# Kernel tuning notes

Measured on AMD Instinct MI355X. Metric: run time of the kernel, lower is better.

## Reference

```python
import jax, jax.numpy as jnp
import numpy as np

EPS = 1e-5

def bn_eval(x, p):
    # p: [4, C] = gamma, beta, running_mean, running_var; channel-last broadcast
    g, b, m, v = p[0], p[1], p[2], p[3]
    return (x - m) * (g / jnp.sqrt(v + EPS)) + b

def _bn_params(k, c):
    k1, k2, k3, k4 = jax.random.split(k, 4)
    gamma = jax.random.uniform(k1, (c,)) + 0.5
    beta = jax.random.normal(k2, (c,)) * 0.1
    mean = jax.random.normal(k3, (c,)) * 0.1
    var = jax.random.uniform(k4, (c,)) + 0.5
    return jnp.stack([gamma, beta, mean, var])

def _lin(k, fan_in, fan_out):
    bound = 1.0 / np.sqrt(fan_in)
    kw, kb = jax.random.split(k)
    w = jax.random.uniform(kw, (fan_in, fan_out), minval=-bound, maxval=bound)
    b = jax.random.uniform(kb, (fan_out,), minval=-bound, maxval=bound)
    return w, b

def setup_inputs() -> dict:
    key = jax.random.key(0)
    B, N, S, C, G = 2, 4096, 16, 256, 8
    ks = jax.random.split(key, 20)
    feats = jax.random.normal(ks[0], (B, N, C), dtype=jnp.float32)
    coords = jax.random.normal(ks[1], (B, N, 3), dtype=jnp.float32)
    index = jax.random.randint(ks[2], (B, N, S), 0, N, dtype=jnp.int32)
    wq, bq = _lin(ks[3], C, C); bnq = _bn_params(ks[4], C)
    wk, bk = _lin(ks[5], C, C); bnk = _bn_params(ks[6], C)
    wv, bv = _lin(ks[7], C, C)
    pm_w1, pm_b1 = _lin(ks[8], 3, C); pm_bn = _bn_params(ks[9], C)
    pm_w2, pm_b2 = _lin(ks[10], C, C)
    pb_w1, pb_b1 = _lin(ks[11], 3, C); pb_bn = _bn_params(ks[12], C)
    pb_w2, pb_b2 = _lin(ks[13], C, C)
    we_w1, we_b1 = _lin(ks[14], C, G); we_bn = _bn_params(ks[15], G)
    we_w2, we_b2 = _lin(ks[16], G, G)
    return dict(feats=feats, coords=coords, index=index,
                wq=wq, bq=bq, bnq=bnq, wk=wk, bk=bk, bnk=bnk, wv=wv, bv=bv,
                pm_w1=pm_w1, pm_b1=pm_b1, pm_bn=pm_bn, pm_w2=pm_w2, pm_b2=pm_b2,
                pb_w1=pb_w1, pb_b1=pb_b1, pb_bn=pb_bn, pb_w2=pb_w2, pb_b2=pb_b2,
                we_w1=we_w1, we_b1=we_b1, we_bn=we_bn, we_w2=we_w2, we_b2=we_b2)

def reference(feats, coords, index,
              wq, bq, bnq, wk, bk, bnk, wv, bv,
              pm_w1, pm_b1, pm_bn, pm_w2, pm_b2,
              pb_w1, pb_b1, pb_bn, pb_w2, pb_b2,
              we_w1, we_b1, we_bn, we_w2, we_b2):
    B, N, C = feats.shape
    S = index.shape[2]
    G = we_w1.shape[1]
    q = jax.nn.relu(bn_eval(feats @ wq + bq, bnq))                       # [B,N,C]
    k = jax.nn.relu(bn_eval(feats @ wk + bk, bnk))                       # [B,N,C]
    v = feats @ wv + bv                                                   # [B,N,C]
    idx = index.reshape(B, N * S)
    key_g = jnp.take_along_axis(k, idx[:, :, None], axis=1).reshape(B, N, S, C)
    val_g = jnp.take_along_axis(v, idx[:, :, None], axis=1).reshape(B, N, S, C)
    crd_g = jnp.take_along_axis(coords, idx[:, :, None], axis=1).reshape(B, N, S, 3)
    relation_qk = key_g - q[:, :, None, :]                                # [B,N,S,C]
    pos = coords[:, :, None, :] - crd_g                                   # [B,N,S,3]
    pem = jax.nn.relu(bn_eval(pos @ pm_w1 + pm_b1, pm_bn)) @ pm_w2 + pm_b2
    relation_qk = relation_qk * pem
    peb = jax.nn.relu(bn_eval(pos @ pb_w1 + pb_b1, pb_bn)) @ pb_w2 + pb_b2
    relation_qk = relation_qk + peb
    val_g = val_g + peb
    w = jax.nn.relu(bn_eval(relation_qk @ we_w1 + we_b1, we_bn)) @ we_w2 + we_b2  # [B,N,S,G]
    w = jax.nn.softmax(w, axis=2)                                         # softmax over neighbors
    val_g = val_g.reshape(B, N, S, G, C // G)
    out = jnp.einsum('bnsgi,bnsg->bngi', val_g, w).reshape(B, N, C)
    return out
```

## Files before the change

### kernel.cpp

```cpp
#include <hip/hip_runtime.h>


typedef __attribute__((ext_vector_type(8))) short bf16x8_t;
typedef __attribute__((ext_vector_type(4))) float f32x4_t;

#define BN_EPS 1e-5f

__device__ __forceinline__ float b2f(unsigned int b) {
    union { unsigned int u; float f; } x; x.u = b << 16; return x.f;
}
__device__ __forceinline__ float blo(unsigned int v) {
    union { unsigned int u; float f; } x; x.u = v << 16; return x.f;
}
__device__ __forceinline__ float bhi(unsigned int v) {
    union { unsigned int u; float f; } x; x.u = v & 0xffff0000u; return x.f;
}
__device__ __forceinline__ unsigned int fbits(float f) {
    union { float f; unsigned int u; } x; x.f = f; return x.u;
}
__device__ __forceinline__ unsigned short f2b(float f) {
    unsigned int u = fbits(f);
    return (unsigned short)((u + 0x7fffu + ((u >> 16) & 1u)) >> 16);
}
__device__ __forceinline__ unsigned int f2bpk(float a, float b) {
    unsigned int ua = fbits(a), ub = fbits(b);
    unsigned int ta = ua + 0x7fffu + ((ua >> 16) & 1u);
    unsigned int tb = ub + 0x7fffu + ((ub >> 16) & 1u);
    return (ta >> 16) | (tb & 0xffff0000u);
}
__device__ __forceinline__ unsigned int relpair(unsigned int kb, unsigned int qb,
                                                unsigned int pm_, unsigned int pb_) {
    float r0 = (blo(kb) - blo(qb)) * blo(pm_) + blo(pb_);
    float r1 = (bhi(kb) - bhi(qb)) * bhi(pm_) + bhi(pb_);
    return f2bpk(r0, r1);
}

__global__ __launch_bounds__(256) void k_prep(
    const float* __restrict__ wq, const float* __restrict__ wk,
    const float* __restrict__ wv, const float* __restrict__ pm2,
    const float* __restrict__ pb2, unsigned short* __restrict__ wsT)
{
    __shared__ unsigned short T[32][72];
    const int bid = blockIdx.x;
    const int mat = bid >> 5;
    const int kk  = (bid >> 2) & 7;
    const int ntq = bid & 3;
    const float* s = (mat == 0) ? wq : (mat == 1) ? wk : (mat == 2) ? wv
                     : (mat == 3) ? pm2 : pb2;
    const int t = threadIdx.x;
    {
        int c = t & 63, r0 = t >> 6;
        for (int i = 0; i < 8; ++i) {
            int r = r0 + i * 4;
            T[r][c] = f2b(s[(kk * 32 + r) * 256 + ntq * 64 + c]);
        }
    }
    __syncthreads();
    {
        int seg = t >> 6, lane = t & 63;
        int col = seg * 16 + (lane & 15);
        int kr  = (lane >> 4) * 8;
        unsigned int v[8];
        #pragma unroll
        for (int j = 0; j < 8; ++j) v[j] = T[kr + j][col];
        uint4 o;
        o.x = v[0] | (v[1] << 16);
        o.y = v[2] | (v[3] << 16);
        o.z = v[4] | (v[5] << 16);
        o.w = v[6] | (v[7] << 16);
        *(uint4*)(wsT + mat * 65536 + (ntq * 4 + seg) * 4096 + kk * 512 + lane * 8) = o;
    }
}

__global__ __launch_bounds__(256) void k_qkv(
    const float* __restrict__ feats,
    const unsigned short* __restrict__ wT,
    const float* __restrict__ bq, const float* __restrict__ bnq,
    const float* __restrict__ bk, const float* __restrict__ bnk,
    const float* __restrict__ bv,
    unsigned short* __restrict__ qkv)
{
    __shared__ unsigned short A[32][264];
    const int t    = threadIdx.x;
    const int widx = blockIdx.x >> 8;
    const int mb   = blockIdx.x & 255;

    for (int i = 0; i < 8; ++i) {
        int row = 4 * i + (t >> 6), col = (t & 63) * 4;
        float4 f = *(const float4*)(feats + (mb * 32 + row) * 256 + col);
        *(uint2*)&A[row][col] = make_uint2(f2bpk(f.x, f.y), f2bpk(f.z, f.w));
    }
    __syncthreads();

    const int lane = t & 63, w = t >> 6;
    const int ln15 = lane & 15, quad = lane >> 4;
    const int mt = w & 1, nh = w >> 1;

    bf16x8_t afr[8];
    #pragma unroll
    for (int kk = 0; kk < 8; ++kk)
        afr[kk] = *(const bf16x8_t*)&A[mt * 16 + ln15][kk * 32 + quad * 8];

    const unsigned short* W = wT + widx * 65536;
    const float* bias = (widx == 0) ? bq : (widx == 1) ? bk : bv;
    const float* bn   = (widx == 0) ? bnq : (widx == 1) ? bnk : nullptr;
    unsigned short* dst = qkv + (size_t)widx * 8192 * 256;

    const f32x4_t fzero = {0.f, 0.f, 0.f, 0.f};
    f32x4_t acc[8];
    for (int j = 0; j < 8; ++j) acc[j] = fzero;

    #pragma unroll
    for (int kk = 0; kk < 8; ++kk) {
        #pragma unroll
        for (int j = 0; j < 8; ++j) {
            int nt = nh * 8 + j;
            bf16x8_t bfr = *(const bf16x8_t*)(W + ((nt * 8 + kk) * 64 + lane) * 8);
            acc[j] = __builtin_amdgcn_mfma_f32_16x16x32_bf16(afr[kk], bfr, acc[j], 0, 0, 0);
        }
    }

    float bb[8], sc[8], mu[8], be[8];
    #pragma unroll
    for (int j = 0; j < 8; ++j) {
        int c = (nh * 8 + j) * 16 + ln15;
        bb[j] = bias[c];
        if (bn) {
            sc[j] = bn[c] / sqrtf(bn[768 + c] + BN_EPS);
            be[j] = bn[256 + c];
            mu[j] = bn[512 + c];
        }
    }
    __syncthreads();
    #pragma unroll
    for (int j = 0; j < 8; ++j) {
        int c = (nh * 8 + j) * 16 + ln15;
        float y[4];
        for (int r = 0; r < 4; ++r) {
            y[r] = acc[j][r] + bb[j];
            if (bn) y[r] = fmaxf((y[r] - mu[j]) * sc[j] + be[j], 0.f);
        }
        for (int r = 0; r < 4; r += 2) {
            unsigned int pk = f2bpk(y[r], y[r + 1]);
            A[mt * 16 + quad * 4 + r][c]     = (unsigned short)pk;
            A[mt * 16 + quad * 4 + r + 1][c] = (unsigned short)(pk >> 16);
        }
    }
    __syncthreads();
    {
        int row = t >> 3, cc = (t & 7) * 32;
        #pragma unroll
        for (int j = 0; j < 4; ++j) {
            uint4 v = *(const uint4*)&A[row][cc + 8 * j];
            *(uint4*)(dst + (mb * 32 + row) * 256 + cc + 8 * j) = v;
        }
    }
}

__global__ __launch_bounds__(256, 2) void k_main(
    const float* __restrict__ coords,
    const int*   __restrict__ index,
    const unsigned short* __restrict__ qm,
    const unsigned short* __restrict__ km,
    const unsigned short* __restrict__ vm,
    const unsigned short* __restrict__ pmw2F,
    const unsigned short* __restrict__ pbw2F,
    const float* __restrict__ pm_w1, const float* __restrict__ pm_b1,
    const float* __restrict__ pm_bn, const float* __restrict__ pm_b2,
    const float* __restrict__ pb_w1, const float* __restrict__ pb_b1,
    const float* __restrict__ pb_bn, const float* __restrict__ pb_b2,
    const float* __restrict__ we_w1, const float* __restrict__ we_b1,
    const float* __restrict__ we_bn, const float* __restrict__ we_w2,
    const float* __restrict__ we_b2,
    float* __restrict__ out)
{
    __shared__ unsigned short bufR[64][264];
    __shared__ unsigned short bufP[64][264];
    __shared__ __align__(16) char uni[8448];
    float (*Wpm)[256] = (float(*)[256])uni;
    float (*Wpb)[256] = (float(*)[256])(uni + 4096);
    unsigned short (*we1T)[264] = (unsigned short(*)[264])uni;
    float (*us_)[8] = (float(*)[8])(uni + 4224);
    float (*lg_)[8] = (float(*)[8])(uni + 6272);
    __shared__ float posA[64][4];
    __shared__ float bias2[2][256];
    __shared__ float swe[8], dwe[8], web2[8];
    __shared__ float we2s[8][8];

    const int t  = threadIdx.x;
    const int P0 = blockIdx.x * 4;
    const int b  = P0 >> 12;

    const int m3  = t >> 2;
    const int Pg3 = P0 + (m3 >> 4);
    const int rg3 = (b << 12) + index[Pg3 * 16 + (m3 & 15)];
    const int c3  = (t & 3) * 8;
    uint4 kpre[8];
    {
        const unsigned short* krow = km + rg3 * 256 + c3;
        #pragma unroll
        for (int i = 0; i < 8; ++i) kpre[i] = *(const uint4*)(krow + 32 * i);
    }
    const int p5 = t >> 6, c5 = (t & 63) * 4;
    uint2 vpre[16];
    #pragma unroll
    for (int s = 0; s < 16; ++s) {
        int rgv = (b << 12) + index[(P0 + p5) * 16 + s];
        vpre[s] = *(const uint2*)(vm + rgv * 256 + c5);
    }

    if (t < 64) {
        int p = t >> 4, s = t & 15;
        int Pg = P0 + p;
        int rg = (b << 12) + index[Pg * 16 + s];
        posA[t][0] = coords[Pg * 3 + 0] - coords[rg * 3 + 0];
        posA[t][1] = coords[Pg * 3 + 1] - coords[rg * 3 + 1];
        posA[t][2] = coords[Pg * 3 + 2] - coords[rg * 3 + 2];
        posA[t][3] = 0.f;
    }
    {
        int c = t;
        float sc = pm_bn[c] / sqrtf(pm_bn[768 + c] + BN_EPS);
        Wpm[0][c] = pm_w1[c] * sc;
        Wpm[1][c] = pm_w1[256 + c] * sc;
        Wpm[2][c] = pm_w1[512 + c] * sc;
        Wpm[3][c] = (pm_b1[c] - pm_bn[512 + c]) * sc + pm_bn[256 + c];
        sc = pb_bn[c] / sqrtf(pb_bn[768 + c] + BN_EPS);
        Wpb[0][c] = pb_w1[c] * sc;
        Wpb[1][c] = pb_w1[256 + c] * sc;
        Wpb[2][c] = pb_w1[512 + c] * sc;
        Wpb[3][c] = (pb_b1[c] - pb_bn[512 + c]) * sc + pb_bn[256 + c];
        bias2[0][c] = pb_b2[c];
        bias2[1][c] = pm_b2[c];
    }
    if (t < 8) {
        float sc = we_bn[t] / sqrtf(we_bn[24 + t] + BN_EPS);
        swe[t]  = sc;
        dwe[t]  = (we_b1[t] - we_bn[16 + t]) * sc + we_bn[8 + t];
        web2[t] = we_b2[t];
    }
    if (t < 64) we2s[t >> 3][t & 7] = we_w2[t];
    __syncthreads();

    const int lane = t & 63, w = t >> 6;
    const int ln15 = lane & 15, quad = lane >> 4;
    const int mrow = w * 16 + ln15;
    const f32x4_t fzero = {0.f, 0.f, 0.f, 0.f};

    const int hc = (t & 127) * 2;
    const int hm0 = (t >> 7) * 32;

    {
        float w00 = Wpb[0][hc], w01 = Wpb[0][hc + 1];
        float w10 = Wpb[1][hc], w11 = Wpb[1][hc + 1];
        float w20 = Wpb[2][hc], w21 = Wpb[2][hc + 1];
        float w30 = Wpb[3][hc], w31 = Wpb[3][hc + 1];
        for (int i = 0; i < 32; ++i) {
            int m = hm0 + i;
            float4 p = *(const float4*)&posA[m][0];
            float h0 = fmaxf(p.x * w00 + p.y * w10 + p.z * w20 + w30, 0.f);
            float h1 = fmaxf(p.x * w01 + p.y * w11 + p.z * w21 + w31, 0.f);
            *(unsigned int*)&bufR[m][hc] = f2bpk(h0, h1);
        }
    }
    __syncthreads();

    f32x4_t acc[4][4];
    for (int a = 0; a < 4; ++a) for (int mt = 0; mt < 4; ++mt) acc[a][mt] = fzero;
    #pragma unroll
    for (int kk = 0; kk < 8; ++kk) {
        bf16x8_t afr[4];
        #pragma unroll
        for (int mt = 0; mt < 4; ++mt)
            afr[mt] = *(const bf16x8_t*)&bufR[mt * 16 + ln15][kk * 32 + quad * 8];
        #pragma unroll
        for (int ntl = 0; ntl < 4; ++ntl) {
            int nt = w * 4 + ntl;
            bf16x8_t bfr = *(const bf16x8_t*)(pbw2F + ((nt * 8 + kk) * 64 + lane) * 8);
            #pragma unroll
            for (int mt = 0; mt < 4; ++mt)
                acc[ntl][mt] = __builtin_amdgcn_mfma_f32_16x16x32_bf16(afr[mt], bfr, acc[ntl][mt], 0, 0, 0);
        }
    }
    __syncthreads();
    #pragma unroll
    for (int ntl = 0; ntl < 4; ++ntl) {
        int c = (w * 4 + ntl) * 16 + ln15;
        float bb = bias2[0][c];
        for (int mt = 0; mt < 4; ++mt)
            for (int r = 0; r < 4; r += 2) {
                unsigned int pk = f2bpk(acc[ntl][mt][r] + bb, acc[ntl][mt][r + 1] + bb);
                bufP[mt * 16 + quad * 4 + r][c]     = (unsigned short)pk;
                bufP[mt * 16 + quad * 4 + r + 1][c] = (unsigned short)(pk >> 16);
            }
    }
    {
        float w00 = Wpm[0][hc], w01 = Wpm[0][hc + 1];
        float w10 = Wpm[1][hc], w11 = Wpm[1][hc + 1];
        float w20 = Wpm[2][hc], w21 = Wpm[2][hc + 1];
        float w30 = Wpm[3][hc], w31 = Wpm[3][hc + 1];
        for (int i = 0; i < 32; ++i) {
            int m = hm0 + i;
            float4 p = *(const float4*)&posA[m][0];
            float h0 = fmaxf(p.x * w00 + p.y * w10 + p.z * w20 + w30, 0.f);
            float h1 = fmaxf(p.x * w01 + p.y * w11 + p.z * w21 + w31, 0.f);
            *(unsigned int*)&bufR[m][hc] = f2bpk(h0, h1);
        }
    }
    __syncthreads();

    for (int a = 0; a < 4; ++a) for (int mt = 0; mt < 4; ++mt) acc[a][mt] = fzero;
    #pragma unroll
    for (int kk = 0; kk < 8; ++kk) {
        bf16x8_t afr[4];
        #pragma unroll
        for (int mt = 0; mt < 4; ++mt)
            afr[mt] = *(const bf16x8_t*)&bufR[mt * 16 + ln15][kk * 32 + quad * 8];
        #pragma unroll
        for (int ntl = 0; ntl < 4; ++ntl) {
            int nt = w * 4 + ntl;
            bf16x8_t bfr = *(const bf16x8_t*)(pmw2F + ((nt * 8 + kk) * 64 + lane) * 8);
            #pragma unroll
            for (int mt = 0; mt < 4; ++mt)
                acc[ntl][mt] = __builtin_amdgcn_mfma_f32_16x16x32_bf16(afr[mt], bfr, acc[ntl][mt], 0, 0, 0);
        }
    }
    __syncthreads();
    #pragma unroll
    for (int ntl = 0; ntl < 4; ++ntl) {
        int c = (w * 4 + ntl) * 16 + ln15;
        float bb = bias2[1][c];
        for (int mt = 0; mt < 4; ++mt)
            for (int r = 0; r < 4; r += 2) {
                unsigned int pk = f2bpk(acc[ntl][mt][r] + bb, acc[ntl][mt][r + 1] + bb);
                bufR[mt * 16 + quad * 4 + r][c]     = (unsigned short)pk;
                bufR[mt * 16 + quad * 4 + r + 1][c] = (unsigned short)(pk >> 16);
            }
    }
    __syncthreads();

    if (t < 64) {
        int g = t >> 3, j8 = t & 7;
        for (int i = 0; i < 32; ++i) {
            int c = j8 * 32 + i;
            we1T[g][c] = f2b(we_w1[c * 8 + g]);
        }
    }
    {
        const unsigned short* qrow = qm + Pg3 * 256 + c3;
        #pragma unroll
        for (int i = 0; i < 8; ++i) {
            int c = c3 + 32 * i;
            uint4 qb  = *(const uint4*)(qrow + 32 * i);
            uint4 pmv = *(const uint4*)&bufR[m3][c];
            uint4 pbv = *(const uint4*)&bufP[m3][c];
            uint4 r;
            r.x = relpair(kpre[i].x, qb.x, pmv.x, pbv.x);
            r.y = relpair(kpre[i].y, qb.y, pmv.y, pbv.y);
            r.z = relpair(kpre[i].z, qb.z, pmv.z, pbv.z);
            r.w = relpair(kpre[i].w, qb.w, pmv.w, pbv.w);
            *(uint4*)&bufR[m3][c] = r;
        }
    }
    __syncthreads();

    {
        const bf16x8_t bz = {0, 0, 0, 0, 0, 0, 0, 0};
        f32x4_t lacc = fzero;
        #pragma unroll
        for (int kk = 0; kk < 8; ++kk) {
            bf16x8_t afr = *(const bf16x8_t*)&bufR[mrow][kk * 32 + quad * 8];
            bf16x8_t bfr = bz;
            if (ln15 < 8) bfr = *(const bf16x8_t*)&we1T[ln15][kk * 32 + quad * 8];
            lacc = __builtin_amdgcn_mfma_f32_16x16x32_bf16(afr, bfr, lacc, 0, 0, 0);
        }
        if (ln15 < 8) {
            float sc = swe[ln15], dd = dwe[ln15];
            for (int r = 0; r < 4; ++r)
                us_[w * 16 + quad * 4 + r][ln15] = fmaxf(lacc[r] * sc + dd, 0.f);
        }
    }
    __syncthreads();

    if (t < 64) {
        float uv[8];
        for (int gp = 0; gp < 8; ++gp) uv[gp] = us_[t][gp];
        for (int g = 0; g < 8; ++g) {
            float l = web2[g];
            for (int gp = 0; gp < 8; ++gp) l += uv[gp] * we2s[gp][g];
            lg_[t][g] = l;
        }
    }
    __syncthreads();

    if (t < 32) {
        int p = t >> 3, g = t & 7;
        float mx = -1e30f;
        for (int s = 0; s < 16; ++s) mx = fmaxf(mx, lg_[p * 16 + s][g]);
        float e[16], sum = 0.f;
        for (int s = 0; s < 16; ++s) { e[s] = __expf(lg_[p * 16 + s][g] - mx); sum += e[s]; }
        float inv = 1.f / sum;
        for (int s = 0; s < 16; ++s) lg_[p * 16 + s][g] = e[s] * inv;
    }
    __syncthreads();

    {
        int g = c5 >> 5;
        float a0 = 0.f, a1 = 0.f, a2 = 0.f, a3 = 0.f;
        #pragma unroll
        for (int s = 0; s < 16; ++s) {
            int m = p5 * 16 + s;
            float wv_ = lg_[m][g];
            uint2 v4 = vpre[s];
            uint2 p4 = *(const uint2*)&bufP[m][c5];
            a0 += wv_ * (blo(v4.x) + blo(p4.x));
            a1 += wv_ * (bhi(v4.x) + bhi(p4.x));
            a2 += wv_ * (blo(v4.y) + blo(p4.y));
            a3 += wv_ * (bhi(v4.y) + bhi(p4.y));
        }
        *(float4*)(out + (size_t)(P0 + p5) * 256 + c5) = make_float4(a0, a1, a2, a3);
    }
}

extern "C" void kernel_launch(void* const* d_in, const int* in_sizes, int n_in,
                              void* d_out, int out_size, void* d_ws, size_t ws_size,
                              hipStream_t stream)
{
    const float* feats  = (const float*)d_in[0];
    const float* coords = (const float*)d_in[1];
    const int*   index  = (const int*)d_in[2];
    const float* wq     = (const float*)d_in[3];
    const float* bq     = (const float*)d_in[4];
    const float* bnq    = (const float*)d_in[5];
    const float* wk     = (const float*)d_in[6];
    const float* bk     = (const float*)d_in[7];
    const float* bnk    = (const float*)d_in[8];
    const float* wv     = (const float*)d_in[9];
    const float* bv     = (const float*)d_in[10];
    const float* pm_w1  = (const float*)d_in[11];
    const float* pm_b1  = (const float*)d_in[12];
    const float* pm_bn  = (const float*)d_in[13];
    const float* pm_w2  = (const float*)d_in[14];
    const float* pm_b2  = (const float*)d_in[15];
    const float* pb_w1  = (const float*)d_in[16];
    const float* pb_b1  = (const float*)d_in[17];
    const float* pb_bn  = (const float*)d_in[18];
    const float* pb_w2  = (const float*)d_in[19];
    const float* pb_b2  = (const float*)d_in[20];
    const float* we_w1  = (const float*)d_in[21];
    const float* we_b1  = (const float*)d_in[22];
    const float* we_bn  = (const float*)d_in[23];
    const float* we_w2  = (const float*)d_in[24];
    const float* we_b2  = (const float*)d_in[25];

    unsigned short* qkv = (unsigned short*)d_ws;
    unsigned short* wsT = qkv + (size_t)3 * 8192 * 256;

    const size_t need = ((size_t)3 * 8192 * 256 + (size_t)5 * 65536) * 2;
    if (ws_size < need) {
        hipMemsetAsync(d_out, 0, (size_t)out_size * 4, stream);
        return;
    }

    k_prep<<<160,  256, 0, stream>>>(wq, wk, wv, pm_w2, pb_w2, wsT);
    k_qkv <<<768,  256, 0, stream>>>(feats, wsT, bq, bnq, bk, bnk, bv, qkv);
    k_main<<<2048, 256, 0, stream>>>(coords, index,
                                     qkv,
                                     qkv + (size_t)8192 * 256,
                                     qkv + (size_t)2 * 8192 * 256,
                                     wsT + 3 * 65536,
                                     wsT + 4 * 65536,
                                     pm_w1, pm_b1, pm_bn, pm_b2,
                                     pb_w1, pb_b1, pb_bn, pb_b2,
                                     we_w1, we_b1, we_bn, we_w2, we_b2,
                                     (float*)d_out);
}
```

Measured before the change: 230.2 us.

## Precompute folded BN weights in prep kernel and make k_main tail wave-local

The folded BN first-layer weights and the transposed bf16 we_w1 are now computed once in extra k_prep blocks and stored in the workspace, so each k_main block no longer rebuilds them in shared memory. Work in k_main is regrouped so each wave owns one point's 16 neighbor rows. The relation computation feeds the MFMA directly from registers instead of going through a shared-memory round trip. The softmax and aggregation tail uses wave-local lgkmcnt waits instead of block barriers, and the value gather moves from an upfront register prefetch to loads inside the final loop. This cuts per-block setup, barriers and register pressure, at the cost of loads that are less overlapped and reliance on the waitcnt being enough for intra-wave LDS ordering.

```diff
diff --git a/kernel.cpp b/kernel.cpp
--- a/kernel.cpp
+++ b/kernel.cpp
@@ -5,10 +5,8 @@
 typedef __attribute__((ext_vector_type(4))) float f32x4_t;
 
 #define BN_EPS 1e-5f
-
-__device__ __forceinline__ float b2f(unsigned int b) {
-    union { unsigned int u; float f; } x; x.u = b << 16; return x.f;
-}
+#define WSYNC() asm volatile("s_waitcnt lgkmcnt(0)" ::: "memory")
+
 __device__ __forceinline__ float blo(unsigned int v) {
     union { unsigned int u; float f; } x; x.u = v << 16; return x.f;
 }
@@ -38,37 +36,61 @@
 __global__ __launch_bounds__(256) void k_prep(
     const float* __restrict__ wq, const float* __restrict__ wk,
     const float* __restrict__ wv, const float* __restrict__ pm2,
-    const float* __restrict__ pb2, unsigned short* __restrict__ wsT)
+    const float* __restrict__ pb2,
+    const float* __restrict__ pm_w1, const float* __restrict__ pm_b1,
+    const float* __restrict__ pm_bn,
+    const float* __restrict__ pb_w1, const float* __restrict__ pb_b1,
+    const float* __restrict__ pb_bn,
+    const float* __restrict__ we_w1,
+    unsigned short* __restrict__ wsT, float* __restrict__ W4,
+    unsigned short* __restrict__ we1TF)
 {
-    __shared__ unsigned short T[32][72];
-    const int bid = blockIdx.x;
-    const int mat = bid >> 5;
-    const int kk  = (bid >> 2) & 7;
-    const int ntq = bid & 3;
-    const float* s = (mat == 0) ? wq : (mat == 1) ? wk : (mat == 2) ? wv
-                     : (mat == 3) ? pm2 : pb2;
-    const int t = threadIdx.x;
-    {
-        int c = t & 63, r0 = t >> 6;
-        for (int i = 0; i < 8; ++i) {
-            int r = r0 + i * 4;
-            T[r][c] = f2b(s[(kk * 32 + r) * 256 + ntq * 64 + c]);
-        }
-    }
-    __syncthreads();
-    {
-        int seg = t >> 6, lane = t & 63;
-        int col = seg * 16 + (lane & 15);
-        int kr  = (lane >> 4) * 8;
-        unsigned int v[8];
-        #pragma unroll
-        for (int j = 0; j < 8; ++j) v[j] = T[kr + j][col];
-        uint4 o;
-        o.x = v[0] | (v[1] << 16);
-        o.y = v[2] | (v[3] << 16);
-        o.z = v[4] | (v[5] << 16);
-        o.w = v[6] | (v[7] << 16);
-        *(uint4*)(wsT + mat * 65536 + (ntq * 4 + seg) * 4096 + kk * 512 + lane * 8) = o;
+    const int bid = blockIdx.x, t = threadIdx.x;
+    if (bid < 160) {
+        __shared__ unsigned short T[32][72];
+        const int mat = bid >> 5;
+        const int kk  = (bid >> 2) & 7;
+        const int ntq = bid & 3;
+        const float* s = (mat == 0) ? wq : (mat == 1) ? wk : (mat == 2) ? wv
+                         : (mat == 3) ? pm2 : pb2;
+        {
+            int c = t & 63, r0 = t >> 6;
+            for (int i = 0; i < 8; ++i) {
+                int r = r0 + i * 4;
+                T[r][c] = f2b(s[(kk * 32 + r) * 256 + ntq * 64 + c]);
+            }
+        }
+        __syncthreads();
+        {
+            int seg = t >> 6, lane = t & 63;
+            int col = seg * 16 + (lane & 15);
+            int kr  = (lane >> 4) * 8;
+            unsigned int v[8];
+            #pragma unroll
+            for (int j = 0; j < 8; ++j) v[j] = T[kr + j][col];
+            uint4 o;
+            o.x = v[0] | (v[1] << 16);
+            o.y = v[2] | (v[3] << 16);
+            o.z = v[4] | (v[5] << 16);
+            o.w = v[6] | (v[7] << 16);
+            *(uint4*)(wsT + mat * 65536 + (ntq * 4 + seg) * 4096 + kk * 512 + lane * 8) = o;
+        }
+    } else if (bid == 160) {
+        int c = t;
+        float s = pm_bn[c] / sqrtf(pm_bn[768 + c] + BN_EPS);
+        float4 wm = make_float4(pm_w1[c] * s, pm_w1[256 + c] * s, pm_w1[512 + c] * s,
+                                (pm_b1[c] - pm_bn[512 + c]) * s + pm_bn[256 + c]);
+        s = pb_bn[c] / sqrtf(pb_bn[768 + c] + BN_EPS);
+        float4 wb = make_float4(pb_w1[c] * s, pb_w1[256 + c] * s, pb_w1[512 + c] * s,
+                                (pb_b1[c] - pb_bn[512 + c]) * s + pb_bn[256 + c]);
+        ((float4*)W4)[c]       = wm;
+        ((float4*)W4)[256 + c] = wb;
+    } else {
+        for (int j = 0; j < 8; ++j) {
+            int e = t * 8 + j;
+            int g = e >> 8, c = e & 255;
+            we1TF[g * 256 + c] = f2b(we_w1[c * 8 + g]);
+        }
     }
 }
 
@@ -165,103 +187,68 @@
     const unsigned short* __restrict__ vm,
     const unsigned short* __restrict__ pmw2F,
     const unsigned short* __restrict__ pbw2F,
-    const float* __restrict__ pm_w1, const float* __restrict__ pm_b1,
-    const float* __restrict__ pm_bn, const float* __restrict__ pm_b2,
-    const float* __restrict__ pb_w1, const float* __restrict__ pb_b1,
-    const float* __restrict__ pb_bn, const float* __restrict__ pb_b2,
-    const float* __restrict__ we_w1, const float* __restrict__ we_b1,
-    const float* __restrict__ we_bn, const float* __restrict__ we_w2,
-    const float* __restrict__ we_b2,
+    const float* __restrict__ W4,
+    const unsigned short* __restrict__ we1TF,
+    const float* __restrict__ pm_b2, const float* __restrict__ pb_b2,
+    const float* __restrict__ we_b1, const float* __restrict__ we_bn,
+    const float* __restrict__ we_w2, const float* __restrict__ we_b2,
     float* __restrict__ out)
 {
     __shared__ unsigned short bufR[64][264];
     __shared__ unsigned short bufP[64][264];
-    __shared__ __align__(16) char uni[8448];
-    float (*Wpm)[256] = (float(*)[256])uni;
-    float (*Wpb)[256] = (float(*)[256])(uni + 4096);
-    unsigned short (*we1T)[264] = (unsigned short(*)[264])uni;
-    float (*us_)[8] = (float(*)[8])(uni + 4224);
-    float (*lg_)[8] = (float(*)[8])(uni + 6272);
     __shared__ float posA[64][4];
-    __shared__ float bias2[2][256];
-    __shared__ float swe[8], dwe[8], web2[8];
+    __shared__ float us_[64][8];
+    __shared__ int   rowg_[64];
     __shared__ float we2s[8][8];
+    __shared__ float web2[8];
 
     const int t  = threadIdx.x;
     const int P0 = blockIdx.x * 4;
-    const int b  = P0 >> 12;
-
-    const int m3  = t >> 2;
-    const int Pg3 = P0 + (m3 >> 4);
-    const int rg3 = (b << 12) + index[Pg3 * 16 + (m3 & 15)];
-    const int c3  = (t & 3) * 8;
+    const int bb_ = P0 >> 12;
+    const int w = t >> 6, lane = t & 63;
+    const int ln15 = lane & 15, quad = lane >> 4;
+    const int R0 = w * 16;
+    const int Pg = P0 + w;
+
+    const int rg = (bb_ << 12) + index[Pg * 16 + ln15];
     uint4 kpre[8];
-    {
-        const unsigned short* krow = km + rg3 * 256 + c3;
-        #pragma unroll
-        for (int i = 0; i < 8; ++i) kpre[i] = *(const uint4*)(krow + 32 * i);
-    }
-    const int p5 = t >> 6, c5 = (t & 63) * 4;
-    uint2 vpre[16];
-    #pragma unroll
-    for (int s = 0; s < 16; ++s) {
-        int rgv = (b << 12) + index[(P0 + p5) * 16 + s];
-        vpre[s] = *(const uint2*)(vm + rgv * 256 + c5);
-    }
-
-    if (t < 64) {
-        int p = t >> 4, s = t & 15;
-        int Pg = P0 + p;
-        int rg = (b << 12) + index[Pg * 16 + s];
-        posA[t][0] = coords[Pg * 3 + 0] - coords[rg * 3 + 0];
-        posA[t][1] = coords[Pg * 3 + 1] - coords[rg * 3 + 1];
-        posA[t][2] = coords[Pg * 3 + 2] - coords[rg * 3 + 2];
-        posA[t][3] = 0.f;
-    }
-    {
-        int c = t;
-        float sc = pm_bn[c] / sqrtf(pm_bn[768 + c] + BN_EPS);
-        Wpm[0][c] = pm_w1[c] * sc;
-        Wpm[1][c] = pm_w1[256 + c] * sc;
-        Wpm[2][c] = pm_w1[512 + c] * sc;
-        Wpm[3][c] = (pm_b1[c] - pm_bn[512 + c]) * sc + pm_bn[256 + c];
-        sc = pb_bn[c] / sqrtf(pb_bn[768 + c] + BN_EPS);
-        Wpb[0][c] = pb_w1[c] * sc;
-        Wpb[1][c] = pb_w1[256 + c] * sc;
-        Wpb[2][c] = pb_w1[512 + c] * sc;
-        Wpb[3][c] = (pb_b1[c] - pb_bn[512 + c]) * sc + pb_bn[256 + c];
-        bias2[0][c] = pb_b2[c];
-        bias2[1][c] = pm_b2[c];
-    }
-    if (t < 8) {
-        float sc = we_bn[t] / sqrtf(we_bn[24 + t] + BN_EPS);
-        swe[t]  = sc;
-        dwe[t]  = (we_b1[t] - we_bn[16 + t]) * sc + we_bn[8 + t];
-        web2[t] = we_b2[t];
+    #pragma unroll
+    for (int kk = 0; kk < 8; ++kk)
+        kpre[kk] = *(const uint4*)(km + rg * 256 + kk * 32 + quad * 8);
+
+    const int hc = lane * 4;
+    float4 cm[4], cb[4];
+    #pragma unroll
+    for (int i = 0; i < 4; ++i) {
+        cm[i] = ((const float4*)W4)[hc + i];
+        cb[i] = ((const float4*)W4)[256 + hc + i];
+    }
+
+    const int g8 = ln15 & 7;
+    const float swe_r = we_bn[g8] / sqrtf(we_bn[24 + g8] + BN_EPS);
+    const float dwe_r = (we_b1[g8] - we_bn[16 + g8]) * swe_r + we_bn[8 + g8];
+
+    if (lane < 16) {
+        rowg_[R0 + lane] = rg;
+        posA[R0 + lane][0] = coords[Pg * 3 + 0] - coords[rg * 3 + 0];
+        posA[R0 + lane][1] = coords[Pg * 3 + 1] - coords[rg * 3 + 1];
+        posA[R0 + lane][2] = coords[Pg * 3 + 2] - coords[rg * 3 + 2];
+        posA[R0 + lane][3] = 0.f;
     }
     if (t < 64) we2s[t >> 3][t & 7] = we_w2[t];
-    __syncthreads();
-
-    const int lane = t & 63, w = t >> 6;
-    const int ln15 = lane & 15, quad = lane >> 4;
-    const int mrow = w * 16 + ln15;
+    if (t < 8)  web2[t] = we_b2[t];
+    WSYNC();
+
     const f32x4_t fzero = {0.f, 0.f, 0.f, 0.f};
 
-    const int hc = (t & 127) * 2;
-    const int hm0 = (t >> 7) * 32;
-
-    {
-        float w00 = Wpb[0][hc], w01 = Wpb[0][hc + 1];
-        float w10 = Wpb[1][hc], w11 = Wpb[1][hc + 1];
-        float w20 = Wpb[2][hc], w21 = Wpb[2][hc + 1];
-        float w30 = Wpb[3][hc], w31 = Wpb[3][hc + 1];
-        for (int i = 0; i < 32; ++i) {
-            int m = hm0 + i;
-            float4 p = *(const float4*)&posA[m][0];
-            float h0 = fmaxf(p.x * w00 + p.y * w10 + p.z * w20 + w30, 0.f);
-            float h1 = fmaxf(p.x * w01 + p.y * w11 + p.z * w21 + w31, 0.f);
-            *(unsigned int*)&bufR[m][hc] = f2bpk(h0, h1);
-        }
+    #pragma unroll
+    for (int m = 0; m < 16; ++m) {
+        float4 p = *(const float4*)&posA[R0 + m][0];
+        float h0 = fmaxf(p.x * cb[0].x + p.y * cb[0].y + p.z * cb[0].z + cb[0].w, 0.f);
+        float h1 = fmaxf(p.x * cb[1].x + p.y * cb[1].y + p.z * cb[1].z + cb[1].w, 0.f);
+        float h2 = fmaxf(p.x * cb[2].x + p.y * cb[2].y + p.z * cb[2].z + cb[2].w, 0.f);
+        float h3 = fmaxf(p.x * cb[3].x + p.y * cb[3].y + p.z * cb[3].z + cb[3].w, 0.f);
+        *(uint2*)&bufR[R0 + m][hc] = make_uint2(f2bpk(h0, h1), f2bpk(h2, h3));
     }
     __syncthreads();
 
@@ -283,29 +270,26 @@
         }
     }
     __syncthreads();
+
     #pragma unroll
     for (int ntl = 0; ntl < 4; ++ntl) {
         int c = (w * 4 + ntl) * 16 + ln15;
-        float bb = bias2[0][c];
+        float bbv = pb_b2[c];
         for (int mt = 0; mt < 4; ++mt)
             for (int r = 0; r < 4; r += 2) {
-                unsigned int pk = f2bpk(acc[ntl][mt][r] + bb, acc[ntl][mt][r + 1] + bb);
+                unsigned int pk = f2bpk(acc[ntl][mt][r] + bbv, acc[ntl][mt][r + 1] + bbv);
                 bufP[mt * 16 + quad * 4 + r][c]     = (unsigned short)pk;
                 bufP[mt * 16 + quad * 4 + r + 1][c] = (unsigned short)(pk >> 16);
             }
     }
-    {
-        float w00 = Wpm[0][hc], w01 = Wpm[0][hc + 1];
-        float w10 = Wpm[1][hc], w11 = Wpm[1][hc + 1];
-        float w20 = Wpm[2][hc], w21 = Wpm[2][hc + 1];
-        float w30 = Wpm[3][hc], w31 = Wpm[3][hc + 1];
-        for (int i = 0; i < 32; ++i) {
-            int m = hm0 + i;
-            float4 p = *(const float4*)&posA[m][0];
-            float h0 = fmaxf(p.x * w00 + p.y * w10 + p.z * w20 + w30, 0.f);
-            float h1 = fmaxf(p.x * w01 + p.y * w11 + p.z * w21 + w31, 0.f);
-            *(unsigned int*)&bufR[m][hc] = f2bpk(h0, h1);
-        }
+    #pragma unroll
+    for (int m = 0; m < 16; ++m) {
+        float4 p = *(const float4*)&posA[R0 + m][0];
+        float h0 = fmaxf(p.x * cm[0].x + p.y * cm[0].y + p.z * cm[0].z + cm[0].w, 0.f);
+        float h1 = fmaxf(p.x * cm[1].x + p.y * cm[1].y + p.z * cm[1].z + cm[1].w, 0.f);
+        float h2 = fmaxf(p.x * cm[2].x + p.y * cm[2].y + p.z * cm[2].z + cm[2].w, 0.f);
+        float h3 = fmaxf(p.x * cm[3].x + p.y * cm[3].y + p.z * cm[3].z + cm[3].w, 0.f);
+        *(uint2*)&bufR[R0 + m][hc] = make_uint2(f2bpk(h0, h1), f2bpk(h2, h3));
     }
     __syncthreads();
 
@@ -326,99 +310,87 @@
         }
     }
     __syncthreads();
+
     #pragma unroll
     for (int ntl = 0; ntl < 4; ++ntl) {
         int c = (w * 4 + ntl) * 16 + ln15;
-        float bb = bias2[1][c];
+        float bbv = pm_b2[c];
         for (int mt = 0; mt < 4; ++mt)
             for (int r = 0; r < 4; r += 2) {
-                unsigned int pk = f2bpk(acc[ntl][mt][r] + bb, acc[ntl][mt][r + 1] + bb);
+                unsigned int pk = f2bpk(acc[ntl][mt][r] + bbv, acc[ntl][mt][r + 1] + bbv);
                 bufR[mt * 16 + quad * 4 + r][c]     = (unsigned short)pk;
                 bufR[mt * 16 + quad * 4 + r + 1][c] = (unsigned short)(pk >> 16);
             }
     }
     __syncthreads();
 
-    if (t < 64) {
-        int g = t >> 3, j8 = t & 7;
-        for (int i = 0; i < 32; ++i) {
-            int c = j8 * 32 + i;
-            we1T[g][c] = f2b(we_w1[c * 8 + g]);
-        }
-    }
-    {
-        const unsigned short* qrow = qm + Pg3 * 256 + c3;
-        #pragma unroll
-        for (int i = 0; i < 8; ++i) {
-            int c = c3 + 32 * i;
-            uint4 qb  = *(const uint4*)(qrow + 32 * i);
-            uint4 pmv = *(const uint4*)&bufR[m3][c];
-            uint4 pbv = *(const uint4*)&bufP[m3][c];
-            uint4 r;
-            r.x = relpair(kpre[i].x, qb.x, pmv.x, pbv.x);
-            r.y = relpair(kpre[i].y, qb.y, pmv.y, pbv.y);
-            r.z = relpair(kpre[i].z, qb.z, pmv.z, pbv.z);
-            r.w = relpair(kpre[i].w, qb.w, pmv.w, pbv.w);
-            *(uint4*)&bufR[m3][c] = r;
-        }
-    }
-    __syncthreads();
-
     {
         const bf16x8_t bz = {0, 0, 0, 0, 0, 0, 0, 0};
         f32x4_t lacc = fzero;
         #pragma unroll
         for (int kk = 0; kk < 8; ++kk) {
-            bf16x8_t afr = *(const bf16x8_t*)&bufR[mrow][kk * 32 + quad * 8];
+            int cb8 = kk * 32 + quad * 8;
+            uint4 pm4 = *(const uint4*)&bufR[R0 + ln15][cb8];
+            uint4 pb4 = *(const uint4*)&bufP[R0 + ln15][cb8];
+            uint4 q4  = *(const uint4*)(qm + Pg * 256 + cb8);
+            union { uint4 u; bf16x8_t v; } rr;
+            rr.u.x = relpair(kpre[kk].x, q4.x, pm4.x, pb4.x);
+            rr.u.y = relpair(kpre[kk].y, q4.y, pm4.y, pb4.y);
+            rr.u.z = relpair(kpre[kk].z, q4.z, pm4.z, pb4.z);
+            rr.u.w = relpair(kpre[kk].w, q4.w, pm4.w, pb4.w);
             bf16x8_t bfr = bz;
-            if (ln15 < 8) bfr = *(const bf16x8_t*)&we1T[ln15][kk * 32 + quad * 8];
-            lacc = __builtin_amdgcn_mfma_f32_16x16x32_bf16(afr, bfr, lacc, 0, 0, 0);
+            if (ln15 < 8) bfr = *(const bf16x8_t*)(we1TF + ln15 * 256 + cb8);
+            lacc = __builtin_amdgcn_mfma_f32_16x16x32_bf16(rr.v, bfr, lacc, 0, 0, 0);
         }
         if (ln15 < 8) {
-            float sc = swe[ln15], dd = dwe[ln15];
+            #pragma unroll
             for (int r = 0; r < 4; ++r)
-                us_[w * 16 + quad * 4 + r][ln15] = fmaxf(lacc[r] * sc + dd, 0.f);
-        }
-    }
-    __syncthreads();
-
-    if (t < 64) {
-        float uv[8];
-        for (int gp = 0; gp < 8; ++gp) uv[gp] = us_[t][gp];
+                us_[R0 + quad * 4 + r][ln15] = fmaxf(lacc[r] * swe_r + dwe_r, 0.f);
+        }
+    }
+    WSYNC();
+
+    if (lane < 16) {
+        float uv[8], l[8];
+        #pragma unroll
+        for (int gp = 0; gp < 8; ++gp) uv[gp] = us_[R0 + lane][gp];
+        #pragma unroll
         for (int g = 0; g < 8; ++g) {
-            float l = web2[g];
-            for (int gp = 0; gp < 8; ++gp) l += uv[gp] * we2s[gp][g];
-            lg_[t][g] = l;
-        }
-    }
-    __syncthreads();
-
-    if (t < 32) {
-        int p = t >> 3, g = t & 7;
+            float x = web2[g];
+            for (int gp = 0; gp < 8; ++gp) x += uv[gp] * we2s[gp][g];
+            l[g] = x;
+        }
+        #pragma unroll
+        for (int g = 0; g < 8; ++g) us_[R0 + lane][g] = l[g];
+    }
+    WSYNC();
+
+    if (lane < 8) {
+        int g = lane;
         float mx = -1e30f;
-        for (int s = 0; s < 16; ++s) mx = fmaxf(mx, lg_[p * 16 + s][g]);
+        for (int s = 0; s < 16; ++s) mx = fmaxf(mx, us_[R0 + s][g]);
         float e[16], sum = 0.f;
-        for (int s = 0; s < 16; ++s) { e[s] = __expf(lg_[p * 16 + s][g] - mx); sum += e[s]; }
+        for (int s = 0; s < 16; ++s) { e[s] = __expf(us_[R0 + s][g] - mx); sum += e[s]; }
         float inv = 1.f / sum;
-        for (int s = 0; s < 16; ++s) lg_[p * 16 + s][g] = e[s] * inv;
-    }
-    __syncthreads();
+        for (int s = 0; s < 16; ++s) us_[R0 + s][g] = e[s] * inv;
+    }
+    WSYNC();
 
     {
-        int g = c5 >> 5;
+        int c5 = lane * 4, g = lane >> 3;
         float a0 = 0.f, a1 = 0.f, a2 = 0.f, a3 = 0.f;
         #pragma unroll
         for (int s = 0; s < 16; ++s) {
-            int m = p5 * 16 + s;
-            float wv_ = lg_[m][g];
-            uint2 v4 = vpre[s];
-            uint2 p4 = *(const uint2*)&bufP[m][c5];
+            int rv = rowg_[R0 + s];
+            float wv_ = us_[R0 + s][g];
+            uint2 v4 = *(const uint2*)(vm + rv * 256 + c5);
+            uint2 p4 = *(const uint2*)&bufP[R0 + s][c5];
             a0 += wv_ * (blo(v4.x) + blo(p4.x));
             a1 += wv_ * (bhi(v4.x) + bhi(p4.x));
             a2 += wv_ * (blo(v4.y) + blo(p4.y));
             a3 += wv_ * (bhi(v4.y) + bhi(p4.y));
         }
-        *(float4*)(out + (size_t)(P0 + p5) * 256 + c5) = make_float4(a0, a1, a2, a3);
+        *(float4*)(out + (size_t)Pg * 256 + c5) = make_float4(a0, a1, a2, a3);
     }
 }
 
@@ -453,16 +425,21 @@
     const float* we_w2  = (const float*)d_in[24];
     const float* we_b2  = (const float*)d_in[25];
 
-    unsigned short* qkv = (unsigned short*)d_ws;
-    unsigned short* wsT = qkv + (size_t)3 * 8192 * 256;
-
-    const size_t need = ((size_t)3 * 8192 * 256 + (size_t)5 * 65536) * 2;
+    unsigned short* qkv   = (unsigned short*)d_ws;
+    unsigned short* wsT   = qkv + (size_t)3 * 8192 * 256;
+    float*          W4    = (float*)(wsT + 5 * 65536);
+    unsigned short* we1TF = (unsigned short*)(W4 + 2048);
+
+    const size_t need = (size_t)13238272 + 8192 + 4096;
     if (ws_size < need) {
         hipMemsetAsync(d_out, 0, (size_t)out_size * 4, stream);
         return;
     }
 
-    k_prep<<<160,  256, 0, stream>>>(wq, wk, wv, pm_w2, pb_w2, wsT);
+    k_prep<<<162,  256, 0, stream>>>(wq, wk, wv, pm_w2, pb_w2,
+                                     pm_w1, pm_b1, pm_bn,
+                                     pb_w1, pb_b1, pb_bn,
+                                     we_w1, wsT, W4, we1TF);
     k_qkv <<<768,  256, 0, stream>>>(feats, wsT, bq, bnq, bk, bnk, bv, qkv);
     k_main<<<2048, 256, 0, stream>>>(coords, index,
                                      qkv,
@@ -470,8 +447,8 @@
                                      qkv + (size_t)2 * 8192 * 256,
                                      wsT + 3 * 65536,
                                      wsT + 4 * 65536,
-                                     pm_w1, pm_b1, pm_bn, pm_b2,
-                                     pb_w1, pb_b1, pb_bn, pb_b2,
-                                     we_w1, we_b1, we_bn, we_w2, we_b2,
+                                     W4, we1TF,
+                                     pm_b2, pb_b2,
+                                     we_b1, we_bn, we_w2, we_b2,
                                      (float*)d_out);
 }
```

New measurement: 206.1 us. 10.5% less time.
